# Kernel optimization log

Hardware: AMD Instinct MI355X
Metric: run time of the kernel (lower is better)

Reference implementation:

```python
import jax, jax.numpy as jnp
import numpy as np

N_NODES = 50000
N_EDGES = 200000
N_GRAPHS = 256
D_IN = 100
H = 384
STEPS = 4
EPS = 1e-5  # torch BatchNorm1d default eps


def setup_inputs() -> dict:
    key = jax.random.key(0)
    ks = jax.random.split(key, 16)
    def nrm(k, shape, s=0.05):
        return jax.random.normal(k, shape, jnp.float32) * s
    return {
        "x": jax.random.normal(ks[0], (N_NODES, D_IN), jnp.float32),
        "edge_index": jax.random.randint(ks[1], (2, N_EDGES), 0, N_NODES, jnp.int32),
        "batch": jnp.sort(jax.random.randint(ks[2], (N_NODES,), 0, N_GRAPHS, jnp.int32)),
        "w_in": nrm(ks[3], (D_IN, H)), "b_in": jnp.zeros((H,), jnp.float32),
        "bn1_g": jnp.ones((H,), jnp.float32), "bn1_b": jnp.zeros((H,), jnp.float32),
        "ggc_w": nrm(ks[4], (STEPS, H, H)),
        "gru_wih": nrm(ks[5], (3 * H, H)), "gru_whh": nrm(ks[6], (3 * H, H)),
        "gru_bih": jnp.zeros((3 * H,), jnp.float32), "gru_bhh": jnp.zeros((3 * H,), jnp.float32),
        "bn2_g": jnp.ones((H,), jnp.float32), "bn2_b": jnp.zeros((H,), jnp.float32),
        "att_w": nrm(ks[7], (H, 1)), "att_b": jnp.zeros((1,), jnp.float32),
        "fc1_w": nrm(ks[8], (H, H)), "fc1_b": jnp.zeros((H,), jnp.float32),
        "bn3_g": jnp.ones((H,), jnp.float32), "bn3_b": jnp.zeros((H,), jnp.float32),
        "fc2_w": nrm(ks[9], (H, H // 2)), "fc2_b": jnp.zeros((H // 2,), jnp.float32),
        "bn4_g": jnp.ones((H // 2,), jnp.float32), "bn4_b": jnp.zeros((H // 2,), jnp.float32),
        "fc3_w": nrm(ks[10], (H // 2, 2)), "fc3_b": jnp.zeros((2,), jnp.float32),
    }


def _bn(x, g, b):
    # training-mode BatchNorm1d: biased batch stats over dim 0
    m = x.mean(0)
    v = x.var(0)
    return (x - m) * jax.lax.rsqrt(v + EPS) * g + b


def reference(x, edge_index, batch, w_in, b_in, bn1_g, bn1_b, ggc_w,
              gru_wih, gru_whh, gru_bih, gru_bhh, bn2_g, bn2_b,
              att_w, att_b, fc1_w, fc1_b, bn3_g, bn3_b,
              fc2_w, fc2_b, bn4_g, bn4_b, fc3_w, fc3_b):
    h = jax.nn.relu(_bn(x @ w_in + b_in, bn1_g, bn1_b))  # [N, H]
    skip = h
    src, dst = edge_index[0], edge_index[1]
    # GatedGraphConv: per-step linear -> scatter-add over edges -> GRUCell
    for i in range(STEPS):
        m = h @ ggc_w[i]                                   # [N, H]
        agg = jax.ops.segment_sum(m[src], dst, num_segments=N_NODES)
        gi = agg @ gru_wih.T + gru_bih                     # [N, 3H]
        gh = h @ gru_whh.T + gru_bhh
        ir, iz, inn = jnp.split(gi, 3, axis=1)
        hr, hz, hn = jnp.split(gh, 3, axis=1)
        r = jax.nn.sigmoid(ir + hr)
        z = jax.nn.sigmoid(iz + hz)
        n = jnp.tanh(inn + r * hn)
        h = (1.0 - z) * n + z * h
    h = jax.nn.relu(_bn(h, bn2_g, bn2_b) + skip)
    # per-graph attention pooling (segment softmax + weighted segment sum)
    logits = (h @ att_w + att_b)[:, 0]                     # [N]
    seg_max = jax.ops.segment_max(logits, batch, num_segments=N_GRAPHS)
    e = jnp.exp(logits - seg_max[batch])
    denom = jax.ops.segment_sum(e, batch, num_segments=N_GRAPHS)
    w = e / denom[batch]
    pooled = jax.ops.segment_sum(w[:, None] * h, batch, num_segments=N_GRAPHS)  # [G, H]
    y = jax.nn.relu(_bn(pooled @ fc1_w + fc1_b, bn3_g, bn3_b))
    y = jax.nn.relu(_bn(y @ fc2_w + fc2_b, bn4_g, bn4_b))
    return y @ fc3_w + fc3_b                               # [G, 2]
```

## Files before the change

### kernel.cpp

```cpp
#include <hip/hip_runtime.h>
#include <math.h>

#define N_NODESC 50000
#define N_EDGESC 200000
#define N_GRAPHSC 256
#define D_INC 100
#define HD 384
#define STEPSC 4
#define BN_EPS 1e-5f

#define FPSCALE 4194304.0f
#define FPINV   (1.0f / 4194304.0f)

#define STATS_ROWS 512
#define STATS_BLOCKS 98

typedef _Float16 h8v __attribute__((ext_vector_type(8)));
typedef _Float16 h4v __attribute__((ext_vector_type(4)));
typedef float f4v __attribute__((ext_vector_type(4)));

static __device__ __forceinline__ float sigmoidf_(float x) { return 1.0f / (1.0f + expf(-x)); }

static __device__ __forceinline__ f4v mfma3(h8v ah, h8v al, h8v bh, h8v bl, f4v c) {
    c = __builtin_amdgcn_mfma_f32_16x16x32_f16(ah, bh, c, 0, 0, 0);
    c = __builtin_amdgcn_mfma_f32_16x16x32_f16(ah, bl, c, 0, 0, 0);
    c = __builtin_amdgcn_mfma_f32_16x16x32_f16(al, bh, c, 0, 0, 0);
    return c;
}

static __device__ __forceinline__ void gload_lds16(const _Float16* g, _Float16* l) {
    __builtin_amdgcn_global_load_lds(
        (const __attribute__((address_space(1))) unsigned int*)g,
        (__attribute__((address_space(3))) unsigned int*)l, 16, 0, 0);
}

static __device__ __forceinline__ int xcd_swz(int orig, int nwg) {
    const int q = nwg >> 3, r = nwg & 7;
    const int xcd = orig & 7, idx = orig >> 3;
    return (xcd < r ? xcd * (q + 1) : r * (q + 1) + (xcd - r) * q) + idx;
}

__global__ __launch_bounds__(256) void gemm64(const float* __restrict__ A,
                                              const float* __restrict__ B,
                                              const float* __restrict__ bias,
                                              float* __restrict__ C,
                                              int M, int K, int N) {
    __shared__ float As[16][68];
    __shared__ float Bs[16][68];
    const int tid = threadIdx.x;
    const int tx = tid & 15, ty = tid >> 4;
    const int m0 = blockIdx.y << 6, n0 = blockIdx.x << 6;
    const int ar = tid >> 2, ac4 = tid & 3;
    const int br = tid >> 4, bc4 = tid & 15;
    float acc[4][4] = {};
    for (int k0 = 0; k0 < K; k0 += 16) {
        float4 av = make_float4(0.f, 0.f, 0.f, 0.f);
        const int arow = m0 + ar, ak = k0 + (ac4 << 2);
        if (arow < M && ak < K) av = *(const float4*)(A + (size_t)arow * K + ak);
        As[(ac4 << 2) + 0][ar] = av.x;
        As[(ac4 << 2) + 1][ar] = av.y;
        As[(ac4 << 2) + 2][ar] = av.z;
        As[(ac4 << 2) + 3][ar] = av.w;
        float4 bv = make_float4(0.f, 0.f, 0.f, 0.f);
        const int bk = k0 + br;
        if (bk < K) bv = *(const float4*)(B + (size_t)bk * N + n0 + (bc4 << 2));
        *(float4*)&Bs[br][bc4 << 2] = bv;
        __syncthreads();
#pragma unroll
        for (int kk = 0; kk < 16; ++kk) {
            const float4 a = *(const float4*)&As[kk][ty << 2];
            const float4 b = *(const float4*)&Bs[kk][tx << 2];
            const float aarr[4] = {a.x, a.y, a.z, a.w};
            const float barr[4] = {b.x, b.y, b.z, b.w};
#pragma unroll
            for (int i = 0; i < 4; ++i)
#pragma unroll
                for (int j = 0; j < 4; ++j) acc[i][j] = fmaf(aarr[i], barr[j], acc[i][j]);
        }
        __syncthreads();
    }
#pragma unroll
    for (int i = 0; i < 4; ++i) {
        const int row = m0 + (ty << 2) + i;
        if (row >= M) continue;
        const int col0 = n0 + (tx << 2);
        float4 out;
        out.x = acc[i][0]; out.y = acc[i][1]; out.z = acc[i][2]; out.w = acc[i][3];
        if (bias) {
            out.x += bias[col0 + 0]; out.y += bias[col0 + 1];
            out.z += bias[col0 + 2]; out.w += bias[col0 + 3];
        }
        *(float4*)(C + (size_t)row * N + col0) = out;
    }
}


__global__ __launch_bounds__(256) void pack_gru_w(const float* __restrict__ w,
                                                  _Float16* __restrict__ PH,
                                                  _Float16* __restrict__ PL) {
    const int i = blockIdx.x * 256 + threadIdx.x;
    if (i >= 3 * 24 * 12 * 64) return;
    const int l = i & 63;
    const int kc = (i >> 6) % 12;
    const int jt = ((i >> 6) / 12) % 24;
    const int g = (i >> 6) / (12 * 24);
    const int row = g * HD + jt * 16 + (l & 15);
    const int k0 = kc * 32 + ((l >> 4) << 3);
    const float* s = w + (size_t)row * HD + k0;
    h8v hi, lo;
#pragma unroll
    for (int e = 0; e < 8; ++e) {
        const float v = s[e];
        hi[e] = (_Float16)v;
        lo[e] = (_Float16)(v - (float)hi[e]);
    }
    *(h8v*)(PH + (size_t)i * 8) = hi;
    *(h8v*)(PL + (size_t)i * 8) = lo;
}

__global__ __launch_bounds__(256) void pack_ggc_w(const float* __restrict__ w,
                                                  _Float16* __restrict__ PH,
                                                  _Float16* __restrict__ PL) {
    const int i = blockIdx.x * 256 + threadIdx.x;
    if (i >= STEPSC * 24 * 12 * 64) return;
    const int l = i & 63;
    const int kc = (i >> 6) % 12;
    const int jt = ((i >> 6) / 12) % 24;
    const int s = (i >> 6) / (12 * 24);
    const int n = jt * 16 + (l & 15);
    const int k0 = kc * 32 + ((l >> 4) << 3);
    h8v hi, lo;
#pragma unroll
    for (int e = 0; e < 8; ++e) {
        const float v = w[((size_t)s * HD + k0 + e) * HD + n];
        hi[e] = (_Float16)v;
        lo[e] = (_Float16)(v - (float)hi[e]);
    }
    *(h8v*)(PH + (size_t)i * 8) = hi;
    *(h8v*)(PL + (size_t)i * 8) = lo;
}

__global__ void deg_count(const int* __restrict__ dst, int* __restrict__ deg) {
    const int e = blockIdx.x * 256 + threadIdx.x;
    if (e < N_EDGESC) atomicAdd(&deg[dst[e]], 1);
}

__global__ __launch_bounds__(1024) void scan_deg(const int* __restrict__ deg,
                                                 int* __restrict__ offs) {
    __shared__ int sums[1024];
    const int t = threadIdx.x;
    const int CH = (N_NODESC + 1023) / 1024;
    const int base = t * CH;
    int s = 0;
    for (int i = 0; i < CH; ++i) {
        const int idx = base + i;
        if (idx < N_NODESC) s += deg[idx];
    }
    sums[t] = s;
    __syncthreads();
    for (int o = 1; o < 1024; o <<= 1) {
        const int v = (t >= o) ? sums[t - o] : 0;
        __syncthreads();
        sums[t] += v;
        __syncthreads();
    }
    int run = (t > 0) ? sums[t - 1] : 0;
    for (int i = 0; i < CH; ++i) {
        const int idx = base + i;
        if (idx < N_NODESC) {
            offs[idx] = run;
            run += deg[idx];
        }
    }
    if (t == 1023) offs[N_NODESC] = run;
}

__global__ void fill_csr(const int* __restrict__ src, const int* __restrict__ dst,
                         const int* __restrict__ offs, int* __restrict__ cursor,
                         int* __restrict__ esrc) {
    const int e = blockIdx.x * 256 + threadIdx.x;
    if (e >= N_EDGESC) return;
    const int d = dst[e];
    const int pos = atomicAdd(&cursor[d], 1);
    esrc[offs[d] + pos] = src[e];
}

__global__ __launch_bounds__(256) void gather_agg_h(const _Float16* __restrict__ mH,
                                                    const _Float16* __restrict__ mL,
                                                    const int* __restrict__ offs,
                                                    const int* __restrict__ esrc,
                                                    _Float16* __restrict__ aggH,
                                                    _Float16* __restrict__ aggL) {
    const int gid = blockIdx.x * 256 + threadIdx.x;
    const int n = gid / 48;
    const int c = gid % 48;
    if (n >= N_NODESC) return;
    const int beg = offs[n], end = offs[n + 1];
    int acc[8] = {};
    for (int i = beg; i < end; ++i) {
        const int s = esrc[i];
        const size_t so = (size_t)s * HD + (c << 3);
        const h8v vh = *(const h8v*)(mH + so);
        const h8v vl = *(const h8v*)(mL + so);
#pragma unroll
        for (int j = 0; j < 8; ++j)
            acc[j] += __float2int_rn(((float)vh[j] + (float)vl[j]) * FPSCALE);
    }
    h8v a, b;
#pragma unroll
    for (int j = 0; j < 8; ++j) {
        const float v = acc[j] * FPINV;
        a[j] = (_Float16)v;
        b[j] = (_Float16)(v - (float)a[j]);
    }
    *(h8v*)(aggH + (size_t)n * HD + (c << 3)) = a;
    *(h8v*)(aggL + (size_t)n * HD + (c << 3)) = b;
}

__global__ __launch_bounds__(256) void ggc_lds(const _Float16* __restrict__ hH,
                                               const _Float16* __restrict__ hL,
                                               const _Float16* __restrict__ wtH,
                                               const _Float16* __restrict__ wtL,
                                               _Float16* __restrict__ mH,
                                               _Float16* __restrict__ mL) {
    __shared__ _Float16 sH[2][2][64][64];
    const int tid = threadIdx.x;
    const int wid = tid >> 6, lane = tid & 63;
    const int lr = lane & 15, lk = lane >> 4;
    const int wr = wid >> 1, wc = wid & 1;
    const int wgid = xcd_swz(blockIdx.x, gridDim.x);
    const int row0 = (wgid / 6) << 6, j0 = (wgid % 6) << 6;
    const int sp = wid >> 1;
    const int srbase = (wid & 1) << 5;
    const int lrow = lane >> 3, ls = lane & 7;
    const _Float16* splane = sp ? hL : hH;

    f4v acc[2][2];
    const f4v z4 = {0.f, 0.f, 0.f, 0.f};
    acc[0][0] = z4; acc[0][1] = z4; acc[1][0] = z4; acc[1][1] = z4;

#define GGC_STAGE(BUF, K0)                                                     \
    _Pragma("unroll")                                                          \
    for (int t4 = 0; t4 < 4; ++t4) {                                           \
        const int row = srbase + (t4 << 3) + lrow;                             \
        const int gk = (K0) + ((ls ^ (row & 7)) << 3);                         \
        const int grow = min(row0 + row, N_NODESC - 1);                        \
        gload_lds16(splane + (size_t)grow * HD + gk,                           \
                    &sH[BUF][sp][srbase + (t4 << 3)][0]);                      \
    }

    GGC_STAGE(0, 0);
    __syncthreads();
    int cur = 0;
    for (int t = 0; t < HD / 64; ++t) {
        if (t + 1 < HD / 64) GGC_STAGE(cur ^ 1, (t + 1) * 64);
#pragma unroll
        for (int kk = 0; kk < 64; kk += 32) {
            h8v fh[2], fl[2], bh[2], bl[2];
#pragma unroll
            for (int sm = 0; sm < 2; ++sm) {
                const int row = wr * 32 + sm * 16 + lr;
                const int s8 = (((kk >> 3) + lk) ^ (row & 7)) << 3;
                fh[sm] = *(const h8v*)&sH[cur][0][row][s8];
                fl[sm] = *(const h8v*)&sH[cur][1][row][s8];
            }
            const int kc = t * 2 + (kk >> 5);
#pragma unroll
            for (int sn = 0; sn < 2; ++sn) {
                const int jt = (j0 >> 4) + wc * 2 + sn;
                const size_t woff = ((size_t)(jt * 12 + kc) << 9) + (lane << 3);
                bh[sn] = *(const h8v*)(wtH + woff);
                bl[sn] = *(const h8v*)(wtL + woff);
            }
            __builtin_amdgcn_s_setprio(1);
#pragma unroll
            for (int sm = 0; sm < 2; ++sm)
#pragma unroll
                for (int sn = 0; sn < 2; ++sn)
                    acc[sm][sn] = mfma3(fh[sm], fl[sm], bh[sn], bl[sn], acc[sm][sn]);
            __builtin_amdgcn_s_setprio(0);
        }
        __syncthreads();
        cur ^= 1;
    }
#pragma unroll
    for (int sm = 0; sm < 2; ++sm)
#pragma unroll
        for (int sn = 0; sn < 2; ++sn) {
            const int col = j0 + wc * 32 + sn * 16 + lr;
#pragma unroll
            for (int j = 0; j < 4; ++j) {
                const int row = row0 + wr * 32 + sm * 16 + lk * 4 + j;
                if (row < N_NODESC) {
                    const size_t off = (size_t)row * HD + col;
                    const float v = acc[sm][sn][j];
                    const _Float16 hh = (_Float16)v;
                    mH[off] = hh;
                    mL[off] = (_Float16)(v - (float)hh);
                }
            }
        }
#undef GGC_STAGE
}

__global__ __launch_bounds__(256) void gru_lds(const _Float16* __restrict__ aH,
                                               const _Float16* __restrict__ aL,
                                               const _Float16* __restrict__ hH,
                                               const _Float16* __restrict__ hL,
                                               const _Float16* __restrict__ wihH,
                                               const _Float16* __restrict__ wihL,
                                               const _Float16* __restrict__ whhH,
                                               const _Float16* __restrict__ whhL,
                                               const float* __restrict__ bih,
                                               const float* __restrict__ bhh,
                                               _Float16* __restrict__ oH,
                                               _Float16* __restrict__ oL) {
    __shared__ _Float16 sA[2][4][64][64];
    const int tid = threadIdx.x;
    const int wid = tid >> 6, lane = tid & 63;
    const int lr = lane & 15, lk = lane >> 4;
    const int wc = wid;
    const int wgid = xcd_swz(blockIdx.x, gridDim.x);
    const int row0 = (wgid / 6) << 6, j0 = (wgid % 6) << 6;
    const int col = j0 + wc * 16 + lr;
    const int tmatch = j0 >> 6;
    const int lrow = lane >> 3, ls = lane & 7;
    const _Float16* splane = (wid == 0) ? aH : (wid == 1) ? aL : (wid == 2) ? hH : hL;

    f4v acc[4][4];
    const f4v z4 = {0.f, 0.f, 0.f, 0.f};
#pragma unroll
    for (int g = 0; g < 4; ++g)
#pragma unroll
        for (int a = 0; a < 4; ++a) acc[g][a] = z4;
    float hold[4][4];

#define GRU_STAGE(BUF, K0)                                                     \
    _Pragma("unroll")                                                          \
    for (int t8 = 0; t8 < 8; ++t8) {                                           \
        const int row = (t8 << 3) + lrow;                                      \
        const int gk = (K0) + ((ls ^ (row & 7)) << 3);                         \
        const int grow = min(row0 + row, N_NODESC - 1);                        \
        gload_lds16(splane + (size_t)grow * HD + gk,                           \
                    &sA[BUF][wid][t8 << 3][0]);                                \
    }

    GRU_STAGE(0, 0);
    __syncthreads();
    int cur = 0;
    for (int t = 0; t < HD / 64; ++t) {
        if (t + 1 < HD / 64) GRU_STAGE(cur ^ 1, (t + 1) * 64);
#pragma unroll
        for (int kk = 0; kk < 64; kk += 32) {
            h8v fAh[4], fAl[4], fHh[4], fHl[4];
#pragma unroll
            for (int sm = 0; sm < 4; ++sm) {
                const int row = sm * 16 + lr;
                const int s8 = (((kk >> 3) + lk) ^ (row & 7)) << 3;
                fAh[sm] = *(const h8v*)&sA[cur][0][row][s8];
                fAl[sm] = *(const h8v*)&sA[cur][1][row][s8];
                fHh[sm] = *(const h8v*)&sA[cur][2][row][s8];
                fHl[sm] = *(const h8v*)&sA[cur][3][row][s8];
            }
            const int kc = t * 2 + (kk >> 5);
            const int jt = (j0 >> 4) + wc;
#pragma unroll
            for (int g = 0; g < 3; ++g) {
                const size_t woff = ((size_t)((g * 24 + jt) * 12 + kc) << 9) + (lane << 3);
                const h8v BiH = *(const h8v*)(wihH + woff);
                const h8v BiL = *(const h8v*)(wihL + woff);
                const h8v BhH = *(const h8v*)(whhH + woff);
                const h8v BhL = *(const h8v*)(whhL + woff);
                __builtin_amdgcn_s_setprio(1);
                if (g < 2) {
#pragma unroll
                    for (int sm = 0; sm < 4; ++sm) {
                        acc[g][sm] = mfma3(fAh[sm], fAl[sm], BiH, BiL, acc[g][sm]);
                        acc[g][sm] = mfma3(fHh[sm], fHl[sm], BhH, BhL, acc[g][sm]);
                    }
                } else {
#pragma unroll
                    for (int sm = 0; sm < 4; ++sm) {
                        acc[2][sm] = mfma3(fAh[sm], fAl[sm], BiH, BiL, acc[2][sm]);
                        acc[3][sm] = mfma3(fHh[sm], fHl[sm], BhH, BhL, acc[3][sm]);
                    }
                }
                __builtin_amdgcn_s_setprio(0);
            }
        }
        if (t == tmatch) {
            const int lc = wc * 16 + lr;
#pragma unroll
            for (int sm = 0; sm < 4; ++sm)
#pragma unroll
                for (int j = 0; j < 4; ++j) {
                    const int row = sm * 16 + lk * 4 + j;
                    const int sc = (((lc >> 3) ^ (row & 7)) << 3) | (lc & 7);
                    hold[sm][j] = (float)sA[cur][2][row][sc] + (float)sA[cur][3][row][sc];
                }
        }
        __syncthreads();
        cur ^= 1;
    }
    const float brz = bih[col] + bhh[col];
    const float bzz = bih[HD + col] + bhh[HD + col];
    const float bni = bih[2 * HD + col];
    const float bnh = bhh[2 * HD + col];
#pragma unroll
    for (int sm = 0; sm < 4; ++sm)
#pragma unroll
        for (int j = 0; j < 4; ++j) {
            const int row = row0 + sm * 16 + lk * 4 + j;
            if (row < N_NODESC) {
                const size_t off = (size_t)row * HD + col;
                const float r = sigmoidf_(acc[0][sm][j] + brz);
                const float z = sigmoidf_(acc[1][sm][j] + bzz);
                const float n = tanhf((acc[2][sm][j] + bni) + r * (acc[3][sm][j] + bnh));
                const float res = (1.f - z) * n + z * hold[sm][j];
                const _Float16 hh = (_Float16)res;
                oH[off] = hh;
                oL[off] = (_Float16)(res - (float)hh);
            }
        }
#undef GRU_STAGE
}

__global__ __launch_bounds__(384) void col_stats_partial(const float* __restrict__ X, int M,
                                                         float* __restrict__ pS,
                                                         float* __restrict__ pQ) {
    const int f = threadIdx.x;
    const int b = blockIdx.x;
    const int r0 = b * STATS_ROWS;
    const int r1 = min(r0 + STATS_ROWS, M);
    float s = 0.f, q = 0.f;
    for (int r = r0; r < r1; ++r) {
        const float v = X[(size_t)r * HD + f];
        s += v;
        q += v * v;
    }
    pS[b * HD + f] = s;
    pQ[b * HD + f] = q;
}

__global__ __launch_bounds__(384) void col_stats_h(const _Float16* __restrict__ hH,
                                                   const _Float16* __restrict__ hL, int M,
                                                   float* __restrict__ pS,
                                                   float* __restrict__ pQ) {
    const int f = threadIdx.x;
    const int b = blockIdx.x;
    const int r0 = b * STATS_ROWS;
    const int r1 = min(r0 + STATS_ROWS, M);
    float s = 0.f, q = 0.f;
    for (int r = r0; r < r1; ++r) {
        const size_t off = (size_t)r * HD + f;
        const float v = (float)hH[off] + (float)hL[off];
        s += v;
        q += v * v;
    }
    pS[b * HD + f] = s;
    pQ[b * HD + f] = q;
}

__global__ void bn_stats_final(const float* __restrict__ pS, const float* __restrict__ pQ,
                               const float* __restrict__ g, const float* __restrict__ b,
                               float* __restrict__ scale, float* __restrict__ shift, float invM) {
    const int f = threadIdx.x;
    float s = 0.f, q = 0.f;
    for (int blk = 0; blk < STATS_BLOCKS; ++blk) {
        s += pS[blk * HD + f];
        q += pQ[blk * HD + f];
    }
    const float mean = s * invM;
    const float var = q * invM - mean * mean;
    const float sc = g[f] * rsqrtf(var + BN_EPS);
    scale[f] = sc;
    shift[f] = b[f] - mean * sc;
}

__global__ __launch_bounds__(256) void bn_relu_split(const float* __restrict__ X,
                                                     const float* __restrict__ scale,
                                                     const float* __restrict__ shift,
                                                     _Float16* __restrict__ hH,
                                                     _Float16* __restrict__ hL) {
    const size_t i4 = (size_t)blockIdx.x * 256 + threadIdx.x;
    const int f = (int)((i4 * 4) % HD);
    const float4 v = ((const float4*)X)[i4];
    float r0 = fmaxf(fmaf(v.x, scale[f + 0], shift[f + 0]), 0.f);
    float r1 = fmaxf(fmaf(v.y, scale[f + 1], shift[f + 1]), 0.f);
    float r2 = fmaxf(fmaf(v.z, scale[f + 2], shift[f + 2]), 0.f);
    float r3 = fmaxf(fmaf(v.w, scale[f + 3], shift[f + 3]), 0.f);
    h4v a, b;
    a[0] = (_Float16)r0; b[0] = (_Float16)(r0 - (float)a[0]);
    a[1] = (_Float16)r1; b[1] = (_Float16)(r1 - (float)a[1]);
    a[2] = (_Float16)r2; b[2] = (_Float16)(r2 - (float)a[2]);
    a[3] = (_Float16)r3; b[3] = (_Float16)(r3 - (float)a[3]);
    *(h4v*)(hH + i4 * 4) = a;
    *(h4v*)(hL + i4 * 4) = b;
}

__global__ __launch_bounds__(256) void bn_skip_relu_h2(const _Float16* __restrict__ hH,
                                                       const _Float16* __restrict__ hL,
                                                       const float* __restrict__ scale,
                                                       const float* __restrict__ shift,
                                                       const float* __restrict__ G,
                                                       const float* __restrict__ scale1,
                                                       const float* __restrict__ shift1,
                                                       float* __restrict__ out) {
    const size_t i4 = (size_t)blockIdx.x * 256 + threadIdx.x;
    const int f = (int)((i4 * 4) % HD);
    const h4v a = *(const h4v*)(hH + i4 * 4);
    const h4v b = *(const h4v*)(hL + i4 * 4);
    const float4 g = ((const float4*)G)[i4];
    const float s0 = fmaxf(fmaf(g.x, scale1[f + 0], shift1[f + 0]), 0.f);
    const float s1 = fmaxf(fmaf(g.y, scale1[f + 1], shift1[f + 1]), 0.f);
    const float s2 = fmaxf(fmaf(g.z, scale1[f + 2], shift1[f + 2]), 0.f);
    const float s3 = fmaxf(fmaf(g.w, scale1[f + 3], shift1[f + 3]), 0.f);
    float4 r;
    r.x = fmaxf(fmaf((float)a[0] + (float)b[0], scale[f + 0], shift[f + 0]) + s0, 0.f);
    r.y = fmaxf(fmaf((float)a[1] + (float)b[1], scale[f + 1], shift[f + 1]) + s1, 0.f);
    r.z = fmaxf(fmaf((float)a[2] + (float)b[2], scale[f + 2], shift[f + 2]) + s2, 0.f);
    r.w = fmaxf(fmaf((float)a[3] + (float)b[3], scale[f + 3], shift[f + 3]) + s3, 0.f);
    ((float4*)out)[i4] = r;
}

__global__ __launch_bounds__(64) void att_logits(const float* __restrict__ h2,
                                                 const float* __restrict__ att_w,
                                                 const float* __restrict__ att_b,
                                                 float* __restrict__ logits) {
    const int n = blockIdx.x;
    const int l = threadIdx.x;
    float acc = 0.f;
#pragma unroll
    for (int k = 0; k < HD; k += 64) acc += h2[(size_t)n * HD + k + l] * att_w[k + l];
#pragma unroll
    for (int o = 32; o > 0; o >>= 1) acc += __shfl_down(acc, o);
    if (l == 0) logits[n] = acc + att_b[0];
}

__global__ void count_graphs(const int* __restrict__ batch, int* __restrict__ counts) {
    const int n = blockIdx.x * 256 + threadIdx.x;
    if (n < N_NODESC) atomicAdd(&counts[batch[n]], 1);
}

__global__ void scan_offsets(const int* __restrict__ counts, int* __restrict__ offs) {
    __shared__ int tmp[N_GRAPHSC];
    const int t = threadIdx.x;
    tmp[t] = counts[t];
    __syncthreads();
    for (int o = 1; o < N_GRAPHSC; o <<= 1) {
        int v = (t >= o) ? tmp[t - o] : 0;
        __syncthreads();
        tmp[t] += v;
        __syncthreads();
    }
    offs[t] = tmp[t] - counts[t];
}

__global__ __launch_bounds__(384) void pool_graphs(const float* __restrict__ h2,
                                                   const float* __restrict__ logits,
                                                   const int* __restrict__ offs,
                                                   const int* __restrict__ counts,
                                                   float* __restrict__ pooled) {
    const int g = blockIdx.x;
    const int t = threadIdx.x;
    const int s = offs[g], c = counts[g], e = s + c;
    __shared__ float red[384];
    float mx = -1e30f;
    for (int n = s + t; n < e; n += 384) mx = fmaxf(mx, logits[n]);
    red[t] = mx;
    __syncthreads();
    if (t < 128) red[t] = fmaxf(red[t], fmaxf(red[t + 128], red[t + 256]));
    __syncthreads();
    for (int w = 64; w > 0; w >>= 1) {
        if (t < w) red[t] = fmaxf(red[t], red[t + w]);
        __syncthreads();
    }
    mx = red[0];
    __syncthreads();
    float sm = 0.f;
    for (int n = s + t; n < e; n += 384) sm += expf(logits[n] - mx);
    red[t] = sm;
    __syncthreads();
    if (t < 128) red[t] += red[t + 128] + red[t + 256];
    __syncthreads();
    for (int w = 64; w > 0; w >>= 1) {
        if (t < w) red[t] += red[t + w];
        __syncthreads();
    }
    const float denom = red[0];
    const float inv = (c > 0) ? 1.0f / denom : 0.0f;
    float acc = 0.f;
    for (int n = s; n < e; ++n) acc += expf(logits[n] - mx) * h2[(size_t)n * HD + t];
    pooled[(size_t)g * HD + t] = acc * inv;
}

__global__ void fc_small(const float* __restrict__ X, const float* __restrict__ W,
                         const float* __restrict__ bias, float* __restrict__ Y,
                         int K, int N) {
    const int m = blockIdx.x;
    const int n = threadIdx.x;
    if (n >= N) return;
    float acc = bias[n];
    for (int k = 0; k < K; ++k) acc += X[m * K + k] * W[k * N + n];
    Y[m * N + n] = acc;
}

__global__ void bn_small_relu(float* X, int M, int N,
                              const float* __restrict__ g, const float* __restrict__ b) {
    const int f = threadIdx.x;
    if (f >= N) return;
    float s = 0.f, q = 0.f;
    for (int r = 0; r < M; ++r) {
        const float v = X[r * N + f];
        s += v;
        q += v * v;
    }
    const float mean = s / M;
    const float var = q / M - mean * mean;
    const float sc = g[f] * rsqrtf(var + BN_EPS);
    const float sh = b[f] - mean * sc;
    for (int r = 0; r < M; ++r) X[r * N + f] = fmaxf(X[r * N + f] * sc + sh, 0.f);
}

extern "C" void kernel_launch(void* const* d_in, const int* in_sizes, int n_in,
                              void* d_out, int out_size, void* d_ws, size_t ws_size,
                              hipStream_t stream) {
    const float* x       = (const float*)d_in[0];
    const int*   eidx    = (const int*)d_in[1];
    const int*   batch   = (const int*)d_in[2];
    const float* w_in    = (const float*)d_in[3];
    const float* b_in    = (const float*)d_in[4];
    const float* bn1_g   = (const float*)d_in[5];
    const float* bn1_b   = (const float*)d_in[6];
    const float* ggc_w   = (const float*)d_in[7];
    const float* gru_wih = (const float*)d_in[8];
    const float* gru_whh = (const float*)d_in[9];
    const float* gru_bih = (const float*)d_in[10];
    const float* gru_bhh = (const float*)d_in[11];
    const float* bn2_g   = (const float*)d_in[12];
    const float* bn2_b   = (const float*)d_in[13];
    const float* att_w   = (const float*)d_in[14];
    const float* att_b   = (const float*)d_in[15];
    const float* fc1_w   = (const float*)d_in[16];
    const float* fc1_b   = (const float*)d_in[17];
    const float* bn3_g   = (const float*)d_in[18];
    const float* bn3_b   = (const float*)d_in[19];
    const float* fc2_w   = (const float*)d_in[20];
    const float* fc2_b   = (const float*)d_in[21];
    const float* bn4_g   = (const float*)d_in[22];
    const float* bn4_b   = (const float*)d_in[23];
    const float* fc3_w   = (const float*)d_in[24];
    const float* fc3_b   = (const float*)d_in[25];

    const int* src = eidx;
    const int* dst = eidx + N_EDGESC;

    const size_t NH = (size_t)N_NODESC * HD;
    char* p = (char*)d_ws;
    float* R0 = (float*)p; p += NH * sizeof(float);
    float* R1 = (float*)p; p += NH * sizeof(float);
    float* Mreg = (float*)p; p += NH * sizeof(float);
    _Float16* wihP_H = (_Float16*)p; p += 3 * HD * HD * sizeof(_Float16);
    _Float16* wihP_L = (_Float16*)p; p += 3 * HD * HD * sizeof(_Float16);
    _Float16* whhP_H = (_Float16*)p; p += 3 * HD * HD * sizeof(_Float16);
    _Float16* whhP_L = (_Float16*)p; p += 3 * HD * HD * sizeof(_Float16);
    _Float16* ggcP_H = (_Float16*)p; p += (size_t)STEPSC * HD * HD * sizeof(_Float16);
    _Float16* ggcP_L = (_Float16*)p; p += (size_t)STEPSC * HD * HD * sizeof(_Float16);
    float* logits = (float*)p; p += N_NODESC * sizeof(float);
    float* pS = (float*)p; p += STATS_BLOCKS * HD * sizeof(float);
    float* pQ = (float*)p; p += STATS_BLOCKS * HD * sizeof(float);
    float* scale  = (float*)p; p += HD * sizeof(float);
    float* shift  = (float*)p; p += HD * sizeof(float);
    float* scale1 = (float*)p; p += HD * sizeof(float);
    float* shift1 = (float*)p; p += HD * sizeof(float);
    float* pooled = (float*)p; p += N_GRAPHSC * HD * sizeof(float);
    float* y1 = (float*)p; p += N_GRAPHSC * HD * sizeof(float);
    float* y2 = (float*)p; p += N_GRAPHSC * (HD / 2) * sizeof(float);
    int* counts = (int*)p; p += N_GRAPHSC * sizeof(int);
    int* offs = (int*)p; p += N_GRAPHSC * sizeof(int);
    int* deg    = (int*)p; p += N_NODESC * sizeof(int);
    int* eoffs  = (int*)p; p += (N_NODESC + 1) * sizeof(int);
    int* cursor = (int*)p; p += N_NODESC * sizeof(int);
    int* esrc   = (int*)p; p += N_EDGESC * sizeof(int);

    const int nwg = (HD / 64) * ((N_NODESC + 63) / 64);
    const int ew_blocks = (int)(NH / 4 / 256);

    hipMemsetAsync(deg, 0, N_NODESC * sizeof(int), stream);
    hipMemsetAsync(cursor, 0, N_NODESC * sizeof(int), stream);
    deg_count<<<(N_EDGESC + 255) / 256, 256, 0, stream>>>(dst, deg);
    scan_deg<<<1, 1024, 0, stream>>>(deg, eoffs);
    fill_csr<<<(N_EDGESC + 255) / 256, 256, 0, stream>>>(src, dst, eoffs, cursor, esrc);

    pack_gru_w<<<(3 * 24 * 12 * 64 + 255) / 256, 256, 0, stream>>>(gru_wih, wihP_H, wihP_L);
    pack_gru_w<<<(3 * 24 * 12 * 64 + 255) / 256, 256, 0, stream>>>(gru_whh, whhP_H, whhP_L);
    pack_ggc_w<<<(STEPSC * 24 * 12 * 64 + 255) / 256, 256, 0, stream>>>(ggc_w, ggcP_H, ggcP_L);

    gemm64<<<dim3(HD / 64, (N_NODESC + 63) / 64), 256, 0, stream>>>(x, w_in, b_in, R0,
                                                                    N_NODESC, D_INC, HD);
    col_stats_partial<<<STATS_BLOCKS, 384, 0, stream>>>(R0, N_NODESC, pS, pQ);
    bn_stats_final<<<1, 384, 0, stream>>>(pS, pQ, bn1_g, bn1_b, scale1, shift1, 1.0f / N_NODESC);
    bn_relu_split<<<ew_blocks, 256, 0, stream>>>(R0, scale1, shift1, (_Float16*)R1,
                                                 (_Float16*)R1 + NH);

    float* Hcur = R1;
    float* Oth = R0;
    _Float16* aggH = (_Float16*)Mreg;
    _Float16* aggL = aggH + NH;
    for (int s7 = 0; s7 < STEPSC; ++s7) {
        const _Float16* hcH = (const _Float16*)Hcur;
        const _Float16* hcL = (const _Float16*)Hcur + NH;
        _Float16* mH = (_Float16*)Oth;
        _Float16* mL = mH + NH;
        ggc_lds<<<nwg, 256, 0, stream>>>(hcH, hcL,
                                         ggcP_H + (size_t)s7 * HD * HD,
                                         ggcP_L + (size_t)s7 * HD * HD, mH, mL);
        gather_agg_h<<<(N_NODESC * 48) / 256 + 1, 256, 0, stream>>>(mH, mL, eoffs, esrc,
                                                                    aggH, aggL);
        gru_lds<<<nwg, 256, 0, stream>>>(aggH, aggL, hcH, hcL, wihP_H, wihP_L, whhP_H, whhP_L,
                                         gru_bih, gru_bhh, mH, mL);
        float* t = Hcur; Hcur = Oth; Oth = t;
    }

    const _Float16* hfH = (const _Float16*)Hcur;
    const _Float16* hfL = (const _Float16*)Hcur + NH;
    col_stats_h<<<STATS_BLOCKS, 384, 0, stream>>>(hfH, hfL, N_NODESC, pS, pQ);
    bn_stats_final<<<1, 384, 0, stream>>>(pS, pQ, bn2_g, bn2_b, scale, shift, 1.0f / N_NODESC);
    gemm64<<<dim3(HD / 64, (N_NODESC + 63) / 64), 256, 0, stream>>>(x, w_in, b_in, Oth,
                                                                    N_NODESC, D_INC, HD);
    float* hfinal = Mreg;
    bn_skip_relu_h2<<<ew_blocks, 256, 0, stream>>>(hfH, hfL, scale, shift, Oth,
                                                   scale1, shift1, hfinal);

    att_logits<<<N_NODESC, 64, 0, stream>>>(hfinal, att_w, att_b, logits);
    hipMemsetAsync(counts, 0, N_GRAPHSC * sizeof(int), stream);
    count_graphs<<<(N_NODESC + 255) / 256, 256, 0, stream>>>(batch, counts);
    scan_offsets<<<1, N_GRAPHSC, 0, stream>>>(counts, offs);
    pool_graphs<<<N_GRAPHSC, 384, 0, stream>>>(hfinal, logits, offs, counts, pooled);

    fc_small<<<N_GRAPHSC, 384, 0, stream>>>(pooled, fc1_w, fc1_b, y1, HD, HD);
    bn_small_relu<<<1, 384, 0, stream>>>(y1, N_GRAPHSC, HD, bn3_g, bn3_b);
    fc_small<<<N_GRAPHSC, 192, 0, stream>>>(y1, fc2_w, fc2_b, y2, HD, HD / 2);
    bn_small_relu<<<1, 192, 0, stream>>>(y2, N_GRAPHSC, HD / 2, bn4_g, bn4_b);
    fc_small<<<N_GRAPHSC, 64, 0, stream>>>(y2, fc3_w, fc3_b, (float*)d_out, HD / 2, 2);
}
```

Measured before the change: 2.781 ms.

## Halve LDS K-tile to 32 in GGC and GRU kernels, remap GGC warps

Both the GGC linear and GRU GEMM kernels now stage 32-wide K slices instead of 64, which halves shared memory per block (GRU from 64KB to 32KB) so more blocks can be resident per CU. The swizzle is changed to a 4-chunk XOR pattern that fits the narrower rows. The GGC kernel also moves from a 2x2 warp tiling to having each warp cover all 64 rows for one 16-column strip, so the B fragment loaded from global memory is reused across four MFMAs. The cost is twice as many K iterations and barriers, with less prefetch depth per stage.

```diff
diff --git a/kernel.cpp b/kernel.cpp
--- a/kernel.cpp
+++ b/kernel.cpp
@@ -223,81 +223,68 @@
                                                const _Float16* __restrict__ wtL,
                                                _Float16* __restrict__ mH,
                                                _Float16* __restrict__ mL) {
-    __shared__ _Float16 sH[2][2][64][64];
+    __shared__ _Float16 sH[2][2][64][32];
     const int tid = threadIdx.x;
     const int wid = tid >> 6, lane = tid & 63;
     const int lr = lane & 15, lk = lane >> 4;
-    const int wr = wid >> 1, wc = wid & 1;
+    const int wc = wid;
     const int wgid = xcd_swz(blockIdx.x, gridDim.x);
     const int row0 = (wgid / 6) << 6, j0 = (wgid % 6) << 6;
     const int sp = wid >> 1;
     const int srbase = (wid & 1) << 5;
-    const int lrow = lane >> 3, ls = lane & 7;
+    const int lrow = lane >> 2, lch = lane & 3;
     const _Float16* splane = sp ? hL : hH;
 
-    f4v acc[2][2];
+    f4v acc[4];
     const f4v z4 = {0.f, 0.f, 0.f, 0.f};
-    acc[0][0] = z4; acc[0][1] = z4; acc[1][0] = z4; acc[1][1] = z4;
+    acc[0] = z4; acc[1] = z4; acc[2] = z4; acc[3] = z4;
 
 #define GGC_STAGE(BUF, K0)                                                     \
     _Pragma("unroll")                                                          \
-    for (int t4 = 0; t4 < 4; ++t4) {                                           \
-        const int row = srbase + (t4 << 3) + lrow;                             \
-        const int gk = (K0) + ((ls ^ (row & 7)) << 3);                         \
+    for (int t2 = 0; t2 < 2; ++t2) {                                           \
+        const int row = srbase + (t2 << 4) + lrow;                             \
+        const int gk = (K0) + ((lch ^ ((row >> 1) & 3)) << 3);                 \
         const int grow = min(row0 + row, N_NODESC - 1);                        \
         gload_lds16(splane + (size_t)grow * HD + gk,                           \
-                    &sH[BUF][sp][srbase + (t4 << 3)][0]);                      \
+                    &sH[BUF][sp][srbase + (t2 << 4)][0]);                      \
     }
 
     GGC_STAGE(0, 0);
     __syncthreads();
     int cur = 0;
-    for (int t = 0; t < HD / 64; ++t) {
-        if (t + 1 < HD / 64) GGC_STAGE(cur ^ 1, (t + 1) * 64);
-#pragma unroll
-        for (int kk = 0; kk < 64; kk += 32) {
-            h8v fh[2], fl[2], bh[2], bl[2];
-#pragma unroll
-            for (int sm = 0; sm < 2; ++sm) {
-                const int row = wr * 32 + sm * 16 + lr;
-                const int s8 = (((kk >> 3) + lk) ^ (row & 7)) << 3;
-                fh[sm] = *(const h8v*)&sH[cur][0][row][s8];
-                fl[sm] = *(const h8v*)&sH[cur][1][row][s8];
-            }
-            const int kc = t * 2 + (kk >> 5);
-#pragma unroll
-            for (int sn = 0; sn < 2; ++sn) {
-                const int jt = (j0 >> 4) + wc * 2 + sn;
-                const size_t woff = ((size_t)(jt * 12 + kc) << 9) + (lane << 3);
-                bh[sn] = *(const h8v*)(wtH + woff);
-                bl[sn] = *(const h8v*)(wtL + woff);
-            }
-            __builtin_amdgcn_s_setprio(1);
-#pragma unroll
-            for (int sm = 0; sm < 2; ++sm)
-#pragma unroll
-                for (int sn = 0; sn < 2; ++sn)
-                    acc[sm][sn] = mfma3(fh[sm], fl[sm], bh[sn], bl[sn], acc[sm][sn]);
-            __builtin_amdgcn_s_setprio(0);
-        }
+    for (int t = 0; t < HD / 32; ++t) {
+        if (t + 1 < HD / 32) GGC_STAGE(cur ^ 1, (t + 1) * 32);
+        h8v fh[4], fl[4];
+#pragma unroll
+        for (int sm = 0; sm < 4; ++sm) {
+            const int row = sm * 16 + lr;
+            const int sc = (lk ^ ((row >> 1) & 3)) << 3;
+            fh[sm] = *(const h8v*)&sH[cur][0][row][sc];
+            fl[sm] = *(const h8v*)&sH[cur][1][row][sc];
+        }
+        const int jt = (j0 >> 4) + wc;
+        const size_t woff = ((size_t)(jt * 12 + t) << 9) + (lane << 3);
+        const h8v bh = *(const h8v*)(wtH + woff);
+        const h8v bl = *(const h8v*)(wtL + woff);
+        __builtin_amdgcn_s_setprio(1);
+#pragma unroll
+        for (int sm = 0; sm < 4; ++sm) acc[sm] = mfma3(fh[sm], fl[sm], bh, bl, acc[sm]);
+        __builtin_amdgcn_s_setprio(0);
         __syncthreads();
         cur ^= 1;
     }
-#pragma unroll
-    for (int sm = 0; sm < 2; ++sm)
-#pragma unroll
-        for (int sn = 0; sn < 2; ++sn) {
-            const int col = j0 + wc * 32 + sn * 16 + lr;
-#pragma unroll
-            for (int j = 0; j < 4; ++j) {
-                const int row = row0 + wr * 32 + sm * 16 + lk * 4 + j;
-                if (row < N_NODESC) {
-                    const size_t off = (size_t)row * HD + col;
-                    const float v = acc[sm][sn][j];
-                    const _Float16 hh = (_Float16)v;
-                    mH[off] = hh;
-                    mL[off] = (_Float16)(v - (float)hh);
-                }
+    const int col = j0 + wc * 16 + lr;
+#pragma unroll
+    for (int sm = 0; sm < 4; ++sm)
+#pragma unroll
+        for (int j = 0; j < 4; ++j) {
+            const int row = row0 + sm * 16 + lk * 4 + j;
+            if (row < N_NODESC) {
+                const size_t off = (size_t)row * HD + col;
+                const float v = acc[sm][j];
+                const _Float16 hh = (_Float16)v;
+                mH[off] = hh;
+                mL[off] = (_Float16)(v - (float)hh);
             }
         }
 #undef GGC_STAGE
@@ -315,7 +302,7 @@
                                                const float* __restrict__ bhh,
                                                _Float16* __restrict__ oH,
                                                _Float16* __restrict__ oL) {
-    __shared__ _Float16 sA[2][4][64][64];
+    __shared__ _Float16 sA[2][4][64][32];
     const int tid = threadIdx.x;
     const int wid = tid >> 6, lane = tid & 63;
     const int lr = lane & 15, lk = lane >> 4;
@@ -323,8 +310,10 @@
     const int wgid = xcd_swz(blockIdx.x, gridDim.x);
     const int row0 = (wgid / 6) << 6, j0 = (wgid % 6) << 6;
     const int col = j0 + wc * 16 + lr;
-    const int tmatch = j0 >> 6;
-    const int lrow = lane >> 3, ls = lane & 7;
+    const int lc = wc * 16 + lr;
+    const int tmatch = (j0 >> 5) + (lc >> 5);
+    const int lcm = lc & 31;
+    const int lrow = lane >> 2, lch = lane & 3;
     const _Float16* splane = (wid == 0) ? aH : (wid == 1) ? aL : (wid == 2) ? hH : hL;
 
     f4v acc[4][4];
@@ -337,65 +326,60 @@
 
 #define GRU_STAGE(BUF, K0)                                                     \
     _Pragma("unroll")                                                          \
-    for (int t8 = 0; t8 < 8; ++t8) {                                           \
-        const int row = (t8 << 3) + lrow;                                      \
-        const int gk = (K0) + ((ls ^ (row & 7)) << 3);                         \
+    for (int t4 = 0; t4 < 4; ++t4) {                                           \
+        const int row = (t4 << 4) + lrow;                                      \
+        const int gk = (K0) + ((lch ^ ((row >> 1) & 3)) << 3);                 \
         const int grow = min(row0 + row, N_NODESC - 1);                        \
         gload_lds16(splane + (size_t)grow * HD + gk,                           \
-                    &sA[BUF][wid][t8 << 3][0]);                                \
+                    &sA[BUF][wid][t4 << 4][0]);                                \
     }
 
     GRU_STAGE(0, 0);
     __syncthreads();
     int cur = 0;
-    for (int t = 0; t < HD / 64; ++t) {
-        if (t + 1 < HD / 64) GRU_STAGE(cur ^ 1, (t + 1) * 64);
-#pragma unroll
-        for (int kk = 0; kk < 64; kk += 32) {
-            h8v fAh[4], fAl[4], fHh[4], fHl[4];
-#pragma unroll
-            for (int sm = 0; sm < 4; ++sm) {
-                const int row = sm * 16 + lr;
-                const int s8 = (((kk >> 3) + lk) ^ (row & 7)) << 3;
-                fAh[sm] = *(const h8v*)&sA[cur][0][row][s8];
-                fAl[sm] = *(const h8v*)&sA[cur][1][row][s8];
-                fHh[sm] = *(const h8v*)&sA[cur][2][row][s8];
-                fHl[sm] = *(const h8v*)&sA[cur][3][row][s8];
+    for (int t = 0; t < HD / 32; ++t) {
+        if (t + 1 < HD / 32) GRU_STAGE(cur ^ 1, (t + 1) * 32);
+        h8v fAh[4], fAl[4], fHh[4], fHl[4];
+#pragma unroll
+        for (int sm = 0; sm < 4; ++sm) {
+            const int row = sm * 16 + lr;
+            const int sc = (lk ^ ((row >> 1) & 3)) << 3;
+            fAh[sm] = *(const h8v*)&sA[cur][0][row][sc];
+            fAl[sm] = *(const h8v*)&sA[cur][1][row][sc];
+            fHh[sm] = *(const h8v*)&sA[cur][2][row][sc];
+            fHl[sm] = *(const h8v*)&sA[cur][3][row][sc];
+        }
+        const int jt = (j0 >> 4) + wc;
+#pragma unroll
+        for (int g = 0; g < 3; ++g) {
+            const size_t woff = ((size_t)((g * 24 + jt) * 12 + t) << 9) + (lane << 3);
+            const h8v BiH = *(const h8v*)(wihH + woff);
+            const h8v BiL = *(const h8v*)(wihL + woff);
+            const h8v BhH = *(const h8v*)(whhH + woff);
+            const h8v BhL = *(const h8v*)(whhL + woff);
+            __builtin_amdgcn_s_setprio(1);
+            if (g < 2) {
+#pragma unroll
+                for (int sm = 0; sm < 4; ++sm) {
+                    acc[g][sm] = mfma3(fAh[sm], fAl[sm], BiH, BiL, acc[g][sm]);
+                    acc[g][sm] = mfma3(fHh[sm], fHl[sm], BhH, BhL, acc[g][sm]);
+                }
+            } else {
+#pragma unroll
+                for (int sm = 0; sm < 4; ++sm) {
+                    acc[2][sm] = mfma3(fAh[sm], fAl[sm], BiH, BiL, acc[2][sm]);
+                    acc[3][sm] = mfma3(fHh[sm], fHl[sm], BhH, BhL, acc[3][sm]);
+                }
             }
-            const int kc = t * 2 + (kk >> 5);
-            const int jt = (j0 >> 4) + wc;
-#pragma unroll
-            for (int g = 0; g < 3; ++g) {
-                const size_t woff = ((size_t)((g * 24 + jt) * 12 + kc) << 9) + (lane << 3);
-                const h8v BiH = *(const h8v*)(wihH + woff);
-                const h8v BiL = *(const h8v*)(wihL + woff);
-                const h8v BhH = *(const h8v*)(whhH + woff);
-                const h8v BhL = *(const h8v*)(whhL + woff);
-                __builtin_amdgcn_s_setprio(1);
-                if (g < 2) {
-#pragma unroll
-                    for (int sm = 0; sm < 4; ++sm) {
-                        acc[g][sm] = mfma3(fAh[sm], fAl[sm], BiH, BiL, acc[g][sm]);
-                        acc[g][sm] = mfma3(fHh[sm], fHl[sm], BhH, BhL, acc[g][sm]);
-                    }
-                } else {
-#pragma unroll
-                    for (int sm = 0; sm < 4; ++sm) {
-                        acc[2][sm] = mfma3(fAh[sm], fAl[sm], BiH, BiL, acc[2][sm]);
-                        acc[3][sm] = mfma3(fHh[sm], fHl[sm], BhH, BhL, acc[3][sm]);
-                    }
-                }
-                __builtin_amdgcn_s_setprio(0);
-            }
+            __builtin_amdgcn_s_setprio(0);
         }
         if (t == tmatch) {
-            const int lc = wc * 16 + lr;
 #pragma unroll
             for (int sm = 0; sm < 4; ++sm)
 #pragma unroll
                 for (int j = 0; j < 4; ++j) {
                     const int row = sm * 16 + lk * 4 + j;
-                    const int sc = (((lc >> 3) ^ (row & 7)) << 3) | (lc & 7);
+                    const int sc = ((((lcm >> 3) ^ ((row >> 1) & 3)) << 3) | (lcm & 7));
                     hold[sm][j] = (float)sA[cur][2][row][sc] + (float)sA[cur][3][row][sc];
                 }
         }
```

Measured after the change: 2.900 ms. 4.3% more time.
